# Optimization experiments

Measured on AMD Instinct MI355X. Metric: run time of the kernel, lower is better.

Reference implementation:

```python
import jax, jax.numpy as jnp
import numpy as np

LN_EPS = 1e-5

def _layernorm(x, g, b):
    mu = jnp.mean(x, axis=-1, keepdims=True)
    var = jnp.var(x, axis=-1, keepdims=True)
    return (x - mu) * jax.lax.rsqrt(var + LN_EPS) * g + b

def setup_inputs() -> dict:
    key = jax.random.key(0)
    ks = jax.random.split(key, 8)
    B, L, d_atom, d_hid = 8, 128, 256, 32
    return {
        "z":    jax.random.normal(ks[0], (B, L, d_atom), dtype=jnp.float32),
        "W_in": jax.random.normal(ks[1], (d_atom, 2 * d_hid), dtype=jnp.float32) * 0.02,
        "b_in": jnp.zeros((2 * d_hid,), dtype=jnp.float32),
        "ln_g": jnp.ones((2 * d_hid,), dtype=jnp.float32),
        "ln_b": jnp.zeros((2 * d_hid,), dtype=jnp.float32),
        "W1":   jax.random.normal(ks[2], (d_hid * d_hid, 21), dtype=jnp.float32) * 0.02,
        "b1":   jnp.zeros((21,), dtype=jnp.float32),
        "W2":   jax.random.normal(ks[3], (d_hid * d_hid, 30), dtype=jnp.float32) * 0.02,
        "b2":   jnp.zeros((30,), dtype=jnp.float32),
    }

def reference(z, W_in, b_in, ln_g, ln_b, W1, b1, W2, b2):
    # linear_in: Linear -> exact GELU -> LayerNorm
    ab = _layernorm(jax.nn.gelu(z @ W_in + b_in, approximate=False), ln_g, ln_b)
    h = ab.shape[-1] // 2
    a, b = ab[..., :h], ab[..., h:]              # (B, L, h) each
    # Fused bilinear form: outer(a_l, b_m) flattened to h*h, then Linear.
    # Equivalent to materializing (B, L, L, h*h) and matmul, reassociated.
    W1r = W1.reshape(h, h, -1)                   # (h, h, 21)
    W2r = W2.reshape(h, h, -1)                   # (h, h, 30)
    x1 = jnp.einsum('blc,bmd,cdk->blmk', a, b, W1r) + b1  # (B, L, L, 21)
    x2 = jnp.einsum('blc,bmd,cdk->blmk', a, b, W2r) + b2  # (B, L, L, 30)
    return (x1, x2)
```

## Files before the change

### kernel.cpp

```cpp
#include <hip/hip_runtime.h>
#include <hip/hip_bf16.h>
#include <math.h>

#define NB 8
#define NL 128
#define D_ATOM 256
#define DH 32
#define DAB 64
#define K1 21
#define K2 30
#define KT 51
#define ROWS (NB*NL)
#define LN_EPS 1e-5f

#define OUT1_ROW (NL*K1)
#define OUT2_ROW (NL*K2)
#define STAGE_N  (OUT1_ROW + OUT2_ROW)
#define WCAT 1632

typedef __attribute__((ext_vector_type(8))) short bf16x8;
typedef __attribute__((ext_vector_type(4))) float f32x4;

__device__ __forceinline__ unsigned short f2bf(float x) {
    __hip_bfloat16 h = __float2bfloat16(x);
    return *reinterpret_cast<unsigned short*>(&h);
}

__global__ __launch_bounds__(256) void ln_wprep_kernel(
    const float* __restrict__ z, const float* __restrict__ W_in,
    const float* __restrict__ b_in, const float* __restrict__ ln_g,
    const float* __restrict__ ln_b, const float* __restrict__ W1,
    const float* __restrict__ W2, float* __restrict__ a_ws,
    unsigned short* __restrict__ bbf, unsigned short* __restrict__ Wlin)
{
    const int t = threadIdx.x;

    if (blockIdx.x >= 256) {
        const int base = ((int)blockIdx.x - 256) * 4096;
        #pragma unroll
        for (int e = 0; e < 16; ++e) {
            int idx = base + e * 256 + t;
            if (idx < DH * WCAT) {
                int c = idx / WCAT, o = idx - c * WCAT;
                float v = (o < 672) ? W1[c * 672 + o] : W2[c * 960 + (o - 672)];
                Wlin[idx] = f2bf(v);
            }
        }
        return;
    }

    __shared__ float Wl[D_ATOM * DAB];
    __shared__ float zl[4][D_ATOM];
    const int w = t >> 6, j = t & 63;
    const int row0 = blockIdx.x * 4;

    #pragma unroll
    for (int s = 0; s < 16; ++s) {
        int i4 = t + s * 256;
        ((float4*)Wl)[i4] = ((const float4*)W_in)[i4];
    }
    ((float4*)zl)[t] = ((const float4*)(z + (size_t)row0 * D_ATOM))[t];
    __syncthreads();

    float acc = b_in[j];
    #pragma unroll 8
    for (int i = 0; i < D_ATOM; ++i)
        acc = fmaf(zl[w][i], Wl[i * DAB + j], acc);

    float g = 0.5f * acc * (1.0f + erff(acc * 0.70710678118654752f));

    float s = g, sq = g * g;
    #pragma unroll
    for (int msk = 1; msk < 64; msk <<= 1) {
        s  += __shfl_xor(s,  msk, 64);
        sq += __shfl_xor(sq, msk, 64);
    }
    float mu  = s  * (1.0f / 64.0f);
    float var = sq * (1.0f / 64.0f) - mu * mu;
    float y = (g - mu) * rsqrtf(var + LN_EPS) * ln_g[j] + ln_b[j];

    const int row = row0 + w;
    if (j < DH) {
        a_ws[row * DH + j] = y;
    } else {
        const int d = j - DH, m = row & 127, batch = row >> 7;
        bbf[batch * 4096 + ((m >> 4) << 9) +
            ((((m & 15) | ((d >> 3) << 4)) << 3) | (d & 7))] = f2bf(y);
    }
}

__global__ __launch_bounds__(256) void pair_kernel(
    const float* __restrict__ a_ws, const unsigned short* __restrict__ bbf,
    const unsigned short* __restrict__ Wlin, const float* __restrict__ b1v,
    const float* __restrict__ b2v, float* __restrict__ out)
{
    const int row0  = blockIdx.x * 2;
    const int batch = row0 >> 7;
    const int t     = threadIdx.x;
    const int w  = t >> 6, l = t & 63;
    const int lg = l >> 4, li = l & 15;

    __shared__ unsigned short Tf[2 * 4 * 64 * 8];
    __shared__ __align__(16) float stg[2][STAGE_N];
    __shared__ float al[2][DH];

    #pragma unroll
    for (int s = 0; s < 8; ++s)
        ((unsigned int*)Tf)[t + s * 256] = 0u;
    if (t < 2 * DH) al[t >> 5][t & 31] = a_ws[row0 * DH + t];
    __syncthreads();

    {
        float tacc0[7], tacc1[7];
        const unsigned short* wp[7];
        int fidx[7];
        bool val[7];
        #pragma unroll
        for (int s = 0; s < 7; ++s) {
            int o = t + s * 256;
            val[s] = (o < WCAT);
            int oo = val[s] ? o : 0;
            int d, k;
            if (oo < 672) { d = oo / 21; k = oo % 21; }
            else { int o2 = oo - 672; d = o2 / 30; k = 21 + o2 % 30; }
            wp[s] = Wlin + oo;
            fidx[s] = (((k >> 4) * 64 + ((k & 15) | ((d >> 3) << 4))) << 3) | (d & 7);
            tacc0[s] = 0.f; tacc1[s] = 0.f;
        }
        #pragma unroll 4
        for (int c = 0; c < DH; ++c) {
            float ac0 = al[0][c], ac1 = al[1][c];
            #pragma unroll
            for (int s = 0; s < 7; ++s) {
                float wv = __uint_as_float(((unsigned)wp[s][c * WCAT]) << 16);
                tacc0[s] = fmaf(ac0, wv, tacc0[s]);
                tacc1[s] = fmaf(ac1, wv, tacc1[s]);
            }
        }
        #pragma unroll
        for (int s = 0; s < 7; ++s) {
            if (val[s]) {
                Tf[fidx[s]]        = f2bf(tacc0[s]);
                Tf[2048 + fidx[s]] = f2bf(tacc1[s]);
            }
        }
    }
    __syncthreads();

    const int r  = w >> 1;
    const int mh = w & 1;

    bf16x8 afr[4], bfr[4];
    #pragma unroll
    for (int i = 0; i < 4; ++i)
        afr[i] = ((const bf16x8*)bbf)[batch * 512 + (mh * 4 + i) * 64 + l];
    #pragma unroll
    for (int kt = 0; kt < 4; ++kt)
        bfr[kt] = ((const bf16x8*)Tf)[(r * 4 + kt) * 64 + l];

    float bias[4];
    #pragma unroll
    for (int kt = 0; kt < 4; ++kt) {
        int k = kt * 16 + li;
        bias[kt] = (k < K1) ? b1v[k] : (k < KT ? b2v[k - K1] : 0.f);
    }

    #pragma unroll
    for (int i = 0; i < 4; ++i) {
        const int mbase = (mh * 4 + i) * 16 + lg * 4;
        #pragma unroll
        for (int kt = 0; kt < 4; ++kt) {
            f32x4 acc = __builtin_amdgcn_mfma_f32_16x16x32_bf16(
                afr[i], bfr[kt], (f32x4){0.f, 0.f, 0.f, 0.f}, 0, 0, 0);
            const int k = kt * 16 + li;
            if (k < K1) {
                #pragma unroll
                for (int q = 0; q < 4; ++q)
                    stg[r][(mbase + q) * K1 + k] = acc[q] + bias[kt];
            } else if (k < KT) {
                #pragma unroll
                for (int q = 0; q < 4; ++q)
                    stg[r][OUT1_ROW + (mbase + q) * K2 + (k - K1)] = acc[q] + bias[kt];
            }
        }
    }
    __syncthreads();

    #pragma unroll
    for (int rr = 0; rr < 2; ++rr) {
        const int row = row0 + rr;
        float* o1 = out + (size_t)row * OUT1_ROW;
        float* o2 = out + (size_t)ROWS * OUT1_ROW + (size_t)row * OUT2_ROW;
        const float4* s1 = (const float4*)stg[rr];
        const float4* s2 = (const float4*)(stg[rr] + OUT1_ROW);
        for (int i4 = t; i4 < OUT1_ROW / 4; i4 += 256)
            ((float4*)o1)[i4] = s1[i4];
        for (int i4 = t; i4 < OUT2_ROW / 4; i4 += 256)
            ((float4*)o2)[i4] = s2[i4];
    }
}

extern "C" void kernel_launch(void* const* d_in, const int* in_sizes, int n_in,
                              void* d_out, int out_size, void* d_ws, size_t ws_size,
                              hipStream_t stream) {
    const float* z    = (const float*)d_in[0];
    const float* W_in = (const float*)d_in[1];
    const float* b_in = (const float*)d_in[2];
    const float* ln_g = (const float*)d_in[3];
    const float* ln_b = (const float*)d_in[4];
    const float* W1   = (const float*)d_in[5];
    const float* b1   = (const float*)d_in[6];
    const float* W2   = (const float*)d_in[7];
    const float* b2   = (const float*)d_in[8];
    float* out = (float*)d_out;

    float*          a_ws = (float*)d_ws;
    unsigned short* bbf  = (unsigned short*)(a_ws + 32768);
    unsigned short* Wlin = bbf + 32768;

    ln_wprep_kernel<<<269, 256, 0, stream>>>(z, W_in, b_in, ln_g, ln_b,
                                             W1, W2, a_ws, bbf, Wlin);
    pair_kernel<<<ROWS / 2, 256, 0, stream>>>(a_ws, bbf, Wlin, b1, b2, out);
}
```

Baseline: 23.15 us.

## Interleave bf16 weights per thread and halve pair-kernel staging LDS

The weight-prep blocks now pack the concatenated W1/W2 bf16 weights so that each thread's seven output columns sit in one 16-byte uint4 per input channel. The pair kernel can then fetch them with one vector load instead of seven scalar 16-bit gathers. The output staging buffer is shrunk to a single row: the two row-groups compute and flush in turn, with an extra barrier between them, and launch bounds request 4 blocks per SM. The intent is fewer memory transactions and higher occupancy, paid for with extra synchronisation and serialised MFMA and store phases.

```diff
diff --git a/kernel.cpp b/kernel.cpp
--- a/kernel.cpp
+++ b/kernel.cpp
@@ -31,20 +31,31 @@
     const float* __restrict__ b_in, const float* __restrict__ ln_g,
     const float* __restrict__ ln_b, const float* __restrict__ W1,
     const float* __restrict__ W2, float* __restrict__ a_ws,
-    unsigned short* __restrict__ bbf, unsigned short* __restrict__ Wlin)
+    unsigned short* __restrict__ bbf, unsigned short* __restrict__ Wlin2)
 {
     const int t = threadIdx.x;
 
     if (blockIdx.x >= 256) {
-        const int base = ((int)blockIdx.x - 256) * 4096;
+        const int base = ((int)blockIdx.x - 256) * 512;
         #pragma unroll
-        for (int e = 0; e < 16; ++e) {
-            int idx = base + e * 256 + t;
-            if (idx < DH * WCAT) {
-                int c = idx / WCAT, o = idx - c * WCAT;
-                float v = (o < 672) ? W1[c * 672 + o] : W2[c * 960 + (o - 672)];
-                Wlin[idx] = f2bf(v);
-            }
+        for (int e = 0; e < 2; ++e) {
+            int p  = base + e * 256 + t;
+            int c  = p >> 8, t2 = p & 255;
+            unsigned short v[8];
+            #pragma unroll
+            for (int s = 0; s < 8; ++s) {
+                int o = s * 256 + t2;
+                float val = 0.f;
+                if (o < 672)       val = W1[c * 672 + o];
+                else if (o < WCAT) val = W2[c * 960 + (o - 672)];
+                v[s] = f2bf(val);
+            }
+            uint4 wq;
+            wq.x = (unsigned)v[0] | ((unsigned)v[1] << 16);
+            wq.y = (unsigned)v[2] | ((unsigned)v[3] << 16);
+            wq.z = (unsigned)v[4] | ((unsigned)v[5] << 16);
+            wq.w = (unsigned)v[6] | ((unsigned)v[7] << 16);
+            ((uint4*)Wlin2)[p] = wq;
         }
         return;
     }
@@ -89,9 +100,9 @@
     }
 }
 
-__global__ __launch_bounds__(256) void pair_kernel(
+__global__ __launch_bounds__(256, 4) void pair_kernel(
     const float* __restrict__ a_ws, const unsigned short* __restrict__ bbf,
-    const unsigned short* __restrict__ Wlin, const float* __restrict__ b1v,
+    const unsigned short* __restrict__ Wlin2, const float* __restrict__ b1v,
     const float* __restrict__ b2v, float* __restrict__ out)
 {
     const int row0  = blockIdx.x * 2;
@@ -101,7 +112,7 @@
     const int lg = l >> 4, li = l & 15;
 
     __shared__ unsigned short Tf[2 * 4 * 64 * 8];
-    __shared__ __align__(16) float stg[2][STAGE_N];
+    __shared__ __align__(16) float stg[STAGE_N];
     __shared__ float al[2][DH];
 
     #pragma unroll
@@ -112,7 +123,6 @@
 
     {
         float tacc0[7], tacc1[7];
-        const unsigned short* wp[7];
         int fidx[7];
         bool val[7];
         #pragma unroll
@@ -123,18 +133,26 @@
             int d, k;
             if (oo < 672) { d = oo / 21; k = oo % 21; }
             else { int o2 = oo - 672; d = o2 / 30; k = 21 + o2 % 30; }
-            wp[s] = Wlin + oo;
             fidx[s] = (((k >> 4) * 64 + ((k & 15) | ((d >> 3) << 4))) << 3) | (d & 7);
             tacc0[s] = 0.f; tacc1[s] = 0.f;
         }
+        const uint4* wbase = ((const uint4*)Wlin2) + t;
         #pragma unroll 4
         for (int c = 0; c < DH; ++c) {
             float ac0 = al[0][c], ac1 = al[1][c];
+            uint4 wq = wbase[c * 256];
+            float wv[7];
+            wv[0] = __uint_as_float(wq.x << 16);
+            wv[1] = __uint_as_float(wq.x & 0xffff0000u);
+            wv[2] = __uint_as_float(wq.y << 16);
+            wv[3] = __uint_as_float(wq.y & 0xffff0000u);
+            wv[4] = __uint_as_float(wq.z << 16);
+            wv[5] = __uint_as_float(wq.z & 0xffff0000u);
+            wv[6] = __uint_as_float(wq.w << 16);
             #pragma unroll
             for (int s = 0; s < 7; ++s) {
-                float wv = __uint_as_float(((unsigned)wp[s][c * WCAT]) << 16);
-                tacc0[s] = fmaf(ac0, wv, tacc0[s]);
-                tacc1[s] = fmaf(ac1, wv, tacc1[s]);
+                tacc0[s] = fmaf(ac0, wv[s], tacc0[s]);
+                tacc1[s] = fmaf(ac1, wv[s], tacc1[s]);
             }
         }
         #pragma unroll
@@ -166,37 +184,40 @@
     }
 
     #pragma unroll
-    for (int i = 0; i < 4; ++i) {
-        const int mbase = (mh * 4 + i) * 16 + lg * 4;
-        #pragma unroll
-        for (int kt = 0; kt < 4; ++kt) {
-            f32x4 acc = __builtin_amdgcn_mfma_f32_16x16x32_bf16(
-                afr[i], bfr[kt], (f32x4){0.f, 0.f, 0.f, 0.f}, 0, 0, 0);
-            const int k = kt * 16 + li;
-            if (k < K1) {
+    for (int rr = 0; rr < 2; ++rr) {
+        if (r == rr) {
+            #pragma unroll
+            for (int i = 0; i < 4; ++i) {
+                const int mbase = (mh * 4 + i) * 16 + lg * 4;
                 #pragma unroll
-                for (int q = 0; q < 4; ++q)
-                    stg[r][(mbase + q) * K1 + k] = acc[q] + bias[kt];
-            } else if (k < KT) {
-                #pragma unroll
-                for (int q = 0; q < 4; ++q)
-                    stg[r][OUT1_ROW + (mbase + q) * K2 + (k - K1)] = acc[q] + bias[kt];
-            }
-        }
-    }
-    __syncthreads();
-
-    #pragma unroll
-    for (int rr = 0; rr < 2; ++rr) {
+                for (int kt = 0; kt < 4; ++kt) {
+                    f32x4 acc = __builtin_amdgcn_mfma_f32_16x16x32_bf16(
+                        afr[i], bfr[kt], (f32x4){0.f, 0.f, 0.f, 0.f}, 0, 0, 0);
+                    const int k = kt * 16 + li;
+                    if (k < K1) {
+                        #pragma unroll
+                        for (int q = 0; q < 4; ++q)
+                            stg[(mbase + q) * K1 + k] = acc[q] + bias[kt];
+                    } else if (k < KT) {
+                        #pragma unroll
+                        for (int q = 0; q < 4; ++q)
+                            stg[OUT1_ROW + (mbase + q) * K2 + (k - K1)] = acc[q] + bias[kt];
+                    }
+                }
+            }
+        }
+        __syncthreads();
+
         const int row = row0 + rr;
         float* o1 = out + (size_t)row * OUT1_ROW;
         float* o2 = out + (size_t)ROWS * OUT1_ROW + (size_t)row * OUT2_ROW;
-        const float4* s1 = (const float4*)stg[rr];
-        const float4* s2 = (const float4*)(stg[rr] + OUT1_ROW);
+        const float4* s1 = (const float4*)stg;
+        const float4* s2 = (const float4*)(stg + OUT1_ROW);
         for (int i4 = t; i4 < OUT1_ROW / 4; i4 += 256)
             ((float4*)o1)[i4] = s1[i4];
         for (int i4 = t; i4 < OUT2_ROW / 4; i4 += 256)
             ((float4*)o2)[i4] = s2[i4];
+        if (rr == 0) __syncthreads();
     }
 }
 
@@ -214,11 +235,11 @@
     const float* b2   = (const float*)d_in[8];
     float* out = (float*)d_out;
 
-    float*          a_ws = (float*)d_ws;
-    unsigned short* bbf  = (unsigned short*)(a_ws + 32768);
-    unsigned short* Wlin = bbf + 32768;
-
-    ln_wprep_kernel<<<269, 256, 0, stream>>>(z, W_in, b_in, ln_g, ln_b,
-                                             W1, W2, a_ws, bbf, Wlin);
-    pair_kernel<<<ROWS / 2, 256, 0, stream>>>(a_ws, bbf, Wlin, b1, b2, out);
-}
+    float*          a_ws  = (float*)d_ws;
+    unsigned short* bbf   = (unsigned short*)(a_ws + 32768);
+    unsigned short* Wlin2 = bbf + 32768;
+
+    ln_wprep_kernel<<<272, 256, 0, stream>>>(z, W_in, b_in, ln_g, ln_b,
+                                             W1, W2, a_ws, bbf, Wlin2);
+    pair_kernel<<<ROWS / 2, 256, 0, stream>>>(a_ws, bbf, Wlin2, b1, b2, out);
+}
```

Measured after the change: 22.68 us. -2.0%, faster.
